# Kernel optimization log

Hardware: AMD Instinct MI355X
Metric: run time of the kernel (lower is better)

Reference implementation:

```python
import jax, jax.numpy as jnp
import numpy as np

B, S, D = 2, 2048, 4096
N_Q_HEADS, N_KV_HEADS, HEAD_DIM = 32, 8, 128
N_REP = N_Q_HEADS // N_KV_HEADS
ROPE_THETA = 10000.0


def setup_inputs() -> dict:
    key = jax.random.key(0)
    ks = jax.random.split(key, 5)
    x = jax.random.normal(ks[0], (B, S, D), dtype=jnp.float32)
    sc = 1.0 / np.sqrt(D)
    wq = jax.random.normal(ks[1], (D, N_Q_HEADS * HEAD_DIM), dtype=jnp.float32) * sc
    wk = jax.random.normal(ks[2], (D, N_KV_HEADS * HEAD_DIM), dtype=jnp.float32) * sc
    wv = jax.random.normal(ks[3], (D, N_KV_HEADS * HEAD_DIM), dtype=jnp.float32) * sc
    cache_k = jnp.zeros((B, S, N_KV_HEADS, HEAD_DIM), dtype=jnp.float32)
    cache_v = jnp.zeros((B, S, N_KV_HEADS, HEAD_DIM), dtype=jnp.float32)
    # rotary frequencies: theta_i = 1/ROPE_THETA^(2i/hd), angle = pos * theta_i
    inv_freq = 1.0 / (ROPE_THETA ** (np.arange(0, HEAD_DIM, 2, dtype=np.float32) / HEAD_DIM))
    angles = np.arange(S, dtype=np.float32)[:, None] * inv_freq[None, :]  # [S, hd/2]
    freqs_cos = jnp.asarray(np.cos(angles), dtype=jnp.float32)
    freqs_sin = jnp.asarray(np.sin(angles), dtype=jnp.float32)
    return {"x": x, "wq": wq, "wk": wk, "wv": wv,
            "cache_k": cache_k, "cache_v": cache_v,
            "freqs_cos": freqs_cos, "freqs_sin": freqs_sin,
            "start_pos": 0}


def _apply_rope(x, cos, sin):
    # x: [B, S, H, hd]; cos/sin: [S, hd/2] -> complex rotation of adjacent pairs
    xr = x[..., 0::2]
    xi = x[..., 1::2]
    c = cos[None, :, None, :]
    s = sin[None, :, None, :]
    out_r = xr * c - xi * s
    out_i = xr * s + xi * c
    return jnp.stack([out_r, out_i], axis=-1).reshape(x.shape)


def reference(x, wq, wk, wv, cache_k, cache_v, freqs_cos, freqs_sin, start_pos):
    batch, seq_len, _ = x.shape
    xq = (x @ wq).reshape(batch, seq_len, N_Q_HEADS, HEAD_DIM)
    xk = (x @ wk).reshape(batch, seq_len, N_KV_HEADS, HEAD_DIM)
    xv = (x @ wv).reshape(batch, seq_len, N_KV_HEADS, HEAD_DIM)
    xq = _apply_rope(xq, freqs_cos, freqs_sin)
    xk = _apply_rope(xk, freqs_cos, freqs_sin)
    # KV-cache append
    cache_k = jax.lax.dynamic_update_slice(cache_k, xk, (0, start_pos, 0, 0))
    cache_v = jax.lax.dynamic_update_slice(cache_v, xv, (0, start_pos, 0, 0))
    keys = cache_k[:, : start_pos + seq_len]    # [B, T, Hkv, hd]
    values = cache_v[:, : start_pos + seq_len]
    # GQA: repeat kv heads to match query heads
    keys = jnp.repeat(keys, N_REP, axis=2)      # [B, T, Hq, hd]
    values = jnp.repeat(values, N_REP, axis=2)
    scale = 1.0 / jnp.sqrt(jnp.asarray(HEAD_DIM, dtype=x.dtype))
    scores = jnp.einsum("bqhd,bkhd->bhqk", xq, keys) * scale
    probs = jax.nn.softmax(scores.astype(jnp.float32), axis=-1).astype(xq.dtype)
    out = jnp.einsum("bhqk,bkhd->bqhd", probs, values)
    return out.reshape(batch, seq_len, N_Q_HEADS * HEAD_DIM)
```

## Files before the change

kernel.cpp:

```cpp
#include <hip/hip_runtime.h>

#define BATCH   2
#define S_LEN   2048
#define D_MODEL 4096
#define HD      128
#define NQH     32
#define NKVH    8

typedef unsigned short ushort_t;
typedef __bf16 bf16x8 __attribute__((ext_vector_type(8)));
typedef float floatx4 __attribute__((ext_vector_type(4)));

#define MFMA16(a, b, c) __builtin_amdgcn_mfma_f32_16x16x32_bf16(a, b, c, 0, 0, 0)

#if __has_builtin(__builtin_amdgcn_exp2f)
#define EXP2(x) __builtin_amdgcn_exp2f(x)
#else
#define EXP2(x) __expf((x) * 0.6931471805599453f)
#endif

__device__ __forceinline__ ushort_t f2b(float f) {
    unsigned int x;
    __builtin_memcpy(&x, &f, 4);
    x += 0x7fff + ((x >> 16) & 1);
    return (ushort_t)(x >> 16);
}

__device__ __forceinline__ void gld16(void* lds, const void* g) {
    __builtin_amdgcn_global_load_lds(
        (const __attribute__((address_space(1))) void*)g,
        (__attribute__((address_space(3))) void*)lds, 16, 0, 0);
}

__global__ __launch_bounds__(256) void conv_x(const float* __restrict__ x,
                                              ushort_t* __restrict__ x0,
                                              ushort_t* __restrict__ x1) {
    const size_t i = ((size_t)blockIdx.x * 256 + threadIdx.x) << 2;
    float4 v = *(const float4*)&x[i];
    ushort4 p;
    p.x = f2b(v.x); p.y = f2b(v.y); p.z = f2b(v.z); p.w = f2b(v.w);
    ushort_t* dst = (i < 8388608) ? x0 : x1;
    *(ushort4*)&dst[i & 8388607] = p;
}

__global__ __launch_bounds__(256) void pack_w(const float* __restrict__ wq,
                                              const float* __restrict__ wk,
                                              const float* __restrict__ wv,
                                              ushort_t* __restrict__ WT) {
    __shared__ ushort_t t[64][65];
    const int k0 = blockIdx.x << 6;
    const int n0 = blockIdx.y << 6;
    const float* src;
    int scol, sN;
    if (n0 < 4096)      { src = wq; scol = n0;        sN = 4096; }
    else if (n0 < 5120) { src = wk; scol = n0 - 4096; sN = 1024; }
    else                { src = wv; scol = n0 - 5120; sN = 1024; }
    const int tid = threadIdx.x;
#pragma unroll
    for (int i = 0; i < 16; i++) {
        int idx = tid + (i << 8);
        int r = idx >> 6, c = idx & 63;
        t[r][c] = f2b(src[(size_t)(k0 + r) * sN + scol + c]);
    }
    __syncthreads();
#pragma unroll
    for (int i = 0; i < 16; i++) {
        int idx = tid + (i << 8);
        int r = idx >> 6, c = idx & 63;
        WT[(size_t)(n0 + r) * D_MODEL + k0 + c] = t[c][r];
    }
}

__global__ __launch_bounds__(256) void gemm_qkv(const ushort_t* __restrict__ x0,
                                                const ushort_t* __restrict__ x1,
                                                const ushort_t* __restrict__ WT,
                                                const float* __restrict__ fc,
                                                const float* __restrict__ fs,
                                                ushort_t* __restrict__ Qr,
                                                ushort_t* __restrict__ Kr,
                                                ushort_t* __restrict__ Vt) {
    __shared__ ushort_t At[128 * 64];
    __shared__ ushort_t Bt[128 * 64];
    const int tid  = threadIdx.x;
    const int wid  = tid >> 6;
    const int lane = tid & 63;
    const int bm = blockIdx.y << 7;
    const int bn = blockIdx.x << 7;
    const int wm = (wid & 1) << 6;
    const int wn = (wid >> 1) << 6;

    floatx4 acc[4][4] = {};

    const ushort_t* Xb = (bm < 2048) ? x0 : x1;
    const int bml = bm & 2047;

    const int g = (lane & 7) ^ (lane >> 3);
    const ushort_t* gA = Xb + (size_t)(bml + (wid << 5) + (lane >> 3)) * D_MODEL + (g << 3);
    const ushort_t* gB = WT + (size_t)(bn  + (wid << 5) + (lane >> 3)) * D_MODEL + (g << 3);
    ushort_t* lA = &At[wid << 11];
    ushort_t* lB = &Bt[wid << 11];
    const int l7 = lane & 7;
    const int cl = lane & 15, rg = lane >> 4;

    for (int k0 = 0; k0 < D_MODEL; k0 += 64) {
        __syncthreads();
#pragma unroll
        for (int i = 0; i < 4; i++) {
            gld16(lA + (i << 9), gA + (size_t)(i << 3) * D_MODEL + k0);
            gld16(lB + (i << 9), gB + (size_t)(i << 3) * D_MODEL + k0);
        }
        __syncthreads();
#pragma unroll
        for (int kk = 0; kk < 2; kk++) {
            const int c = (kk << 2) + rg;
            const int slot = (c ^ l7) << 3;
            bf16x8 af[4], bfr[4];
#pragma unroll
            for (int mm = 0; mm < 4; mm++) {
                af[mm]  = *(const bf16x8*)&At[((wm + (mm << 4) + cl) << 6) + slot];
                bfr[mm] = *(const bf16x8*)&Bt[((wn + (mm << 4) + cl) << 6) + slot];
            }
#pragma unroll
            for (int mm = 0; mm < 4; mm++)
#pragma unroll
                for (int nn = 0; nn < 4; nn++)
                    acc[mm][nn] = MFMA16(af[mm], bfr[nn], acc[mm][nn]);
        }
    }

    const int region = blockIdx.x;
    const int b_idx  = bm >> 11;
    const int s0w    = (bm & 2047) + wm;

    if (region < 40) {
        const float oscale = (region < 32)
            ? (0.08838834764831845f * 1.4426950408889634f) : 1.0f;
        ushort_t* dst;
        if (region < 32) dst = Qr + (size_t)(b_idx * NQH  +  region      ) * S_LEN * HD;
        else             dst = Kr + (size_t)(b_idx * NKVH + (region - 32)) * S_LEN * HD;
#pragma unroll
        for (int nn = 0; nn < 4; nn++) {
            const int dcol = wn + (nn << 4) + cl;
            const int d2   = dcol >> 1;
            const float sgn = (dcol & 1) ? 1.0f : -1.0f;
#pragma unroll
            for (int mm = 0; mm < 4; mm++)
#pragma unroll
                for (int r = 0; r < 4; r++) {
                    float v  = acc[mm][nn][r];
                    float pv = __shfl_xor(v, 1);
                    int srow = s0w + (mm << 4) + (rg << 2) + r;
                    float c  = fc[(srow << 6) + d2];
                    float s  = fs[(srow << 6) + d2];
                    float o  = (v * c + sgn * pv * s) * oscale;
                    dst[(size_t)srow * HD + dcol] = f2b(o);
                }
        }
    } else {
        const int kvh = region - 40;
        ushort_t* dst = Vt + (size_t)(b_idx * NKVH + kvh) * HD * S_LEN;
#pragma unroll
        for (int mm = 0; mm < 4; mm++) {
            const int srow = s0w + (mm << 4) + (rg << 2);
#pragma unroll
            for (int nn = 0; nn < 4; nn++) {
                const int dcol = wn + (nn << 4) + cl;
                ushort4 pk;
                pk.x = f2b(acc[mm][nn][0]);
                pk.y = f2b(acc[mm][nn][1]);
                pk.z = f2b(acc[mm][nn][2]);
                pk.w = f2b(acc[mm][nn][3]);
                *(ushort4*)&dst[(size_t)dcol * S_LEN + srow] = pk;
            }
        }
    }
}

__global__ __launch_bounds__(256, 3) void attn(const ushort_t* __restrict__ Qr,
                                               const ushort_t* __restrict__ Kr,
                                               const ushort_t* __restrict__ Vtg,
                                               float* __restrict__ out) {
    __shared__ ushort_t Ktb[2][32 * 128];
    __shared__ ushort_t Vlb[2][128 * 32];
    __shared__ ushort_t Pt[4 * 32 * 40];

    const int tid  = threadIdx.x;
    const int wid  = tid >> 6;
    const int lane = tid & 63;
    const int h  = blockIdx.y;
    const int b  = blockIdx.z;
    const int kh = h >> 2;
    const int q0 = (blockIdx.x << 7) + (wid << 5);

    const int cl = lane & 15, rg = lane >> 4, l7 = lane & 7;

    const ushort_t* Qbase = Qr + ((size_t)(b * NQH + h) * S_LEN + q0 + cl) * HD;
    bf16x8 qf0[4], qf1[4];
#pragma unroll
    for (int dc = 0; dc < 4; dc++) {
        qf0[dc] = *(const bf16x8*)&Qbase[(dc << 5) + (rg << 3)];
        qf1[dc] = *(const bf16x8*)&Qbase[(size_t)16 * HD + (dc << 5) + (rg << 3)];
    }

    floatx4 o0[8] = {}, o1[8] = {};
    float ls0[4] = {0.f, 0.f, 0.f, 0.f};
    float ls1[4] = {0.f, 0.f, 0.f, 0.f};

    const ushort_t* Kb = Kr  + (size_t)(b * NKVH + kh) * S_LEN * HD;
    const ushort_t* Vb = Vtg + (size_t)(b * NKVH + kh) * HD * S_LEN;
    ushort_t* Pw = &Pt[wid * 32 * 40];

    const int vr  = lane >> 2;
    const int gv2 = (lane & 3) ^ (vr & 3);

    auto stage = [&](int bi, int kt0) {
#pragma unroll
        for (int i = 0; i < 2; i++) {
            int ki = (wid << 1) + i;
            gld16(&Ktb[bi][ki << 9],
                  Kb + (size_t)(kt0 + (ki << 2) + rg) * HD
                     + ((cl ^ (((ki & 1) << 2) + rg)) << 3));
            gld16(&Vlb[bi][ki << 9],
                  Vb + (size_t)((ki << 4) + vr) * S_LEN + kt0 + (gv2 << 3));
        }
    };

    stage(0, 0);

#pragma unroll 1
    for (int t = 0; t < 64; t++) {
        if (t < 63) {
            stage((t + 1) & 1, (t + 1) << 5);
            asm volatile("s_waitcnt vmcnt(4)" ::: "memory");
        } else {
            asm volatile("s_waitcnt vmcnt(0)" ::: "memory");
        }
        __builtin_amdgcn_s_barrier();
        asm volatile("" ::: "memory");

        const ushort_t* Kc = Ktb[t & 1];
        const ushort_t* Vc = Vlb[t & 1];

        __builtin_amdgcn_s_setprio(1);
#pragma unroll
        for (int kt = 0; kt < 2; kt++) {
            floatx4 a0 = {0.f, 0.f, 0.f, 0.f};
            floatx4 a1 = {0.f, 0.f, 0.f, 0.f};
#pragma unroll
            for (int dc = 0; dc < 4; dc++) {
                int c = (dc << 2) + rg;
                bf16x8 kf = *(const bf16x8*)
                    &Kc[(((kt << 4) + cl) << 7) + ((c ^ l7) << 3)];
                a0 = MFMA16(qf0[dc], kf, a0);
                a1 = MFMA16(qf1[dc], kf, a1);
            }
#pragma unroll
            for (int r = 0; r < 4; r++) {
                float p0 = EXP2(a0[r]);
                float p1 = EXP2(a1[r]);
                ls0[r] += p0;
                ls1[r] += p1;
                Pw[(((rg << 2) + r)     ) * 40 + (kt << 4) + cl] = f2b(p0);
                Pw[(((rg << 2) + r) + 16) * 40 + (kt << 4) + cl] = f2b(p1);
            }
        }

        {
            bf16x8 pf0 = *(const bf16x8*)&Pw[ cl       * 40 + (rg << 3)];
            bf16x8 pf1 = *(const bf16x8*)&Pw[(cl + 16) * 40 + (rg << 3)];
#pragma unroll
            for (int dt = 0; dt < 8; dt++) {
                int d = (dt << 4) + cl;
                bf16x8 vf = *(const bf16x8*)
                    &Vc[(d << 5) + ((rg ^ (cl & 3)) << 3)];
                o0[dt] = MFMA16(pf0, vf, o0[dt]);
                o1[dt] = MFMA16(pf1, vf, o1[dt]);
            }
        }
        __builtin_amdgcn_s_setprio(0);

        asm volatile("" ::: "memory");
        __builtin_amdgcn_s_barrier();
    }

#pragma unroll
    for (int r = 0; r < 4; r++) {
        float v0 = ls0[r];
        v0 += __shfl_xor(v0, 1);
        v0 += __shfl_xor(v0, 2);
        v0 += __shfl_xor(v0, 4);
        v0 += __shfl_xor(v0, 8);
        ls0[r] = 1.0f / v0;
        float v1 = ls1[r];
        v1 += __shfl_xor(v1, 1);
        v1 += __shfl_xor(v1, 2);
        v1 += __shfl_xor(v1, 4);
        v1 += __shfl_xor(v1, 8);
        ls1[r] = 1.0f / v1;
    }

    float* ob = out + (size_t)(b * S_LEN + q0) * (NQH * HD) + h * HD;
#pragma unroll
    for (int dt = 0; dt < 8; dt++)
#pragma unroll
        for (int r = 0; r < 4; r++) {
            ob[(size_t)((rg << 2) + r) * (NQH * HD) + (dt << 4) + cl] =
                o0[dt][r] * ls0[r];
            ob[(size_t)((rg << 2) + r + 16) * (NQH * HD) + (dt << 4) + cl] =
                o1[dt][r] * ls1[r];
        }
}

extern "C" void kernel_launch(void* const* d_in, const int* in_sizes, int n_in,
                              void* d_out, int out_size, void* d_ws, size_t ws_size,
                              hipStream_t stream) {
    const float* x  = (const float*)d_in[0];
    const float* wq = (const float*)d_in[1];
    const float* wk = (const float*)d_in[2];
    const float* wv = (const float*)d_in[3];
    ushort_t* x0 = (ushort_t*)d_in[4];
    ushort_t* x1 = (ushort_t*)d_in[5];
    const float* fc = (const float*)d_in[6];
    const float* fs = (const float*)d_in[7];
    float* out = (float*)d_out;

    ushort_t* WTx = (ushort_t*)d_in[0];

    char* ws = (char*)d_ws;
    ushort_t* Qr = (ushort_t*)(ws);
    ushort_t* Kr = (ushort_t*)(ws + 33554432);
    ushort_t* Vt = (ushort_t*)(ws + 41943040);

    conv_x  <<<16384,           256, 0, stream>>>(x, x0, x1);
    pack_w  <<<dim3(64, 96),    256, 0, stream>>>(wq, wk, wv, WTx);
    gemm_qkv<<<dim3(48, 32),    256, 0, stream>>>(x0, x1, WTx, fc, fs, Qr, Kr, Vt);
    attn    <<<dim3(16, 32, 2), 256, 0, stream>>>(Qr, Kr, Vt, out);
    (void)in_sizes; (void)n_in; (void)out_size; (void)ws_size;
}
```

Measured before the change: 614.8 us.

## Rewrite QKV GEMM as 256x256 tiles with double-buffered LDS pipeline

The QKV projection GEMM moves from 128x128 tiles with 256 threads to 256x256 tiles with 512 threads (8 waves, each computing 128x64). The LDS buffers are now double-buffered so the next K-slice's global-to-LDS loads are issued in stages while the current slice is being multiplied. Raw barriers, vmcnt waits and s_setprio calls schedule this overlap. The aim is to raise arithmetic intensity and hide memory latency. In exchange it uses 128KB of LDS and many more accumulator registers, and launches only 384 blocks, which reduces occupancy and the number of waves in flight.

```diff
diff --git a/kernel.cpp b/kernel.cpp
--- a/kernel.cpp
+++ b/kernel.cpp
@@ -71,85 +71,168 @@
     }
 }
 
-__global__ __launch_bounds__(256) void gemm_qkv(const ushort_t* __restrict__ x0,
-                                                const ushort_t* __restrict__ x1,
-                                                const ushort_t* __restrict__ WT,
-                                                const float* __restrict__ fc,
-                                                const float* __restrict__ fs,
-                                                ushort_t* __restrict__ Qr,
-                                                ushort_t* __restrict__ Kr,
-                                                ushort_t* __restrict__ Vt) {
-    __shared__ ushort_t At[128 * 64];
-    __shared__ ushort_t Bt[128 * 64];
+__global__ __launch_bounds__(512, 2) void gemm_qkv(const ushort_t* __restrict__ x0,
+                                                   const ushort_t* __restrict__ x1,
+                                                   const ushort_t* __restrict__ WT,
+                                                   const float* __restrict__ fc,
+                                                   const float* __restrict__ fs,
+                                                   ushort_t* __restrict__ Qr,
+                                                   ushort_t* __restrict__ Kr,
+                                                   ushort_t* __restrict__ Vt) {
+    __shared__ ushort_t At[2][256 * 64];
+    __shared__ ushort_t Bt[2][256 * 64];
+
     const int tid  = threadIdx.x;
     const int wid  = tid >> 6;
     const int lane = tid & 63;
-    const int bm = blockIdx.y << 7;
-    const int bn = blockIdx.x << 7;
-    const int wm = (wid & 1) << 6;
-    const int wn = (wid >> 1) << 6;
-
-    floatx4 acc[4][4] = {};
+    const int wm = (wid >> 2) << 7;
+    const int wn = (wid & 3) << 6;
+    const int bm = blockIdx.y << 8;
+    const int bn = blockIdx.x << 8;
+    const int cl = lane & 15, rg = lane >> 4, l7 = lane & 7;
 
     const ushort_t* Xb = (bm < 2048) ? x0 : x1;
     const int bml = bm & 2047;
 
-    const int g = (lane & 7) ^ (lane >> 3);
-    const ushort_t* gA = Xb + (size_t)(bml + (wid << 5) + (lane >> 3)) * D_MODEL + (g << 3);
-    const ushort_t* gB = WT + (size_t)(bn  + (wid << 5) + (lane >> 3)) * D_MODEL + (g << 3);
-    ushort_t* lA = &At[wid << 11];
-    ushort_t* lB = &Bt[wid << 11];
-    const int l7 = lane & 7;
-    const int cl = lane & 15, rg = lane >> 4;
-
-    for (int k0 = 0; k0 < D_MODEL; k0 += 64) {
-        __syncthreads();
+    const int srow8 = tid >> 3;
+    const int gsw   = (tid & 7) ^ (srow8 & 7);
+    const ushort_t* gA = Xb + (size_t)(bml + srow8) * D_MODEL + (gsw << 3);
+    const ushort_t* gB = WT + (size_t)(bn  + srow8) * D_MODEL + (gsw << 3);
+    const int lbase = (wid << 3) << 6;
+
+    floatx4 acc[8][4] = {};
+    bf16x8 af[4][2], bfr[4][2];
+
+    auto stA = [&](int buf, int t, int half) {
+#pragma unroll
+        for (int j = 0; j < 2; j++) {
+            const int row0 = (half << 7) + (j << 6);
+            gld16(&At[buf][(row0 << 6) + lbase],
+                  gA + (size_t)row0 * D_MODEL + ((size_t)t << 6));
+        }
+    };
+    auto stB = [&](int buf, int t, int half) {
+#pragma unroll
+        for (int j = 0; j < 2; j++) {
+            const int row0 = (half << 7) + (j << 6);
+            gld16(&Bt[buf][(row0 << 6) + lbase],
+                  gB + (size_t)row0 * D_MODEL + ((size_t)t << 6));
+        }
+    };
+    auto loadA = [&](const ushort_t* buf, int mh) {
 #pragma unroll
         for (int i = 0; i < 4; i++) {
-            gld16(lA + (i << 9), gA + (size_t)(i << 3) * D_MODEL + k0);
-            gld16(lB + (i << 9), gB + (size_t)(i << 3) * D_MODEL + k0);
-        }
-        __syncthreads();
-#pragma unroll
-        for (int kk = 0; kk < 2; kk++) {
-            const int c = (kk << 2) + rg;
-            const int slot = (c ^ l7) << 3;
-            bf16x8 af[4], bfr[4];
-#pragma unroll
-            for (int mm = 0; mm < 4; mm++) {
-                af[mm]  = *(const bf16x8*)&At[((wm + (mm << 4) + cl) << 6) + slot];
-                bfr[mm] = *(const bf16x8*)&Bt[((wn + (mm << 4) + cl) << 6) + slot];
-            }
-#pragma unroll
-            for (int mm = 0; mm < 4; mm++)
-#pragma unroll
-                for (int nn = 0; nn < 4; nn++)
-                    acc[mm][nn] = MFMA16(af[mm], bfr[nn], acc[mm][nn]);
-        }
-    }
-
-    const int region = blockIdx.x;
+            const int row = wm + (mh << 6) + (i << 4) + cl;
+#pragma unroll
+            for (int kk = 0; kk < 2; kk++)
+                af[i][kk] = *(const bf16x8*)
+                    &buf[(row << 6) + ((((kk << 2) + rg) ^ l7) << 3)];
+        }
+    };
+    auto loadB = [&](const ushort_t* buf) {
+#pragma unroll
+        for (int i = 0; i < 4; i++) {
+            const int row = wn + (i << 4) + cl;
+#pragma unroll
+            for (int kk = 0; kk < 2; kk++)
+                bfr[i][kk] = *(const bf16x8*)
+                    &buf[(row << 6) + ((((kk << 2) + rg) ^ l7) << 3)];
+        }
+    };
+
+    stA(0, 0, 0); stA(0, 0, 1); stB(0, 0, 0); stB(0, 0, 1);
+
+#pragma unroll 1
+    for (int t = 0; t < 64; t++) {
+        const int d = t & 1, e = d ^ 1;
+        const ushort_t* Ad = At[d];
+        const ushort_t* Bd = Bt[d];
+
+        if (t < 63) {
+            stA(e, t + 1, 0); stA(e, t + 1, 1);
+            asm volatile("s_waitcnt vmcnt(4)" ::: "memory");
+        } else {
+            asm volatile("s_waitcnt vmcnt(0)" ::: "memory");
+        }
+        __builtin_amdgcn_s_barrier();
+        asm volatile("" ::: "memory");
+        loadA(Ad, 0);
+        loadB(Bd);
+        __builtin_amdgcn_s_setprio(1);
+#pragma unroll
+        for (int i = 0; i < 4; i++)
+#pragma unroll
+            for (int j = 0; j < 2; j++)
+#pragma unroll
+                for (int kk = 0; kk < 2; kk++)
+                    acc[i][j] = MFMA16(af[i][kk], bfr[j][kk], acc[i][j]);
+        __builtin_amdgcn_s_setprio(0);
+        asm volatile("" ::: "memory");
+        __builtin_amdgcn_s_barrier();
+
+        if (t < 63) stB(e, t + 1, 0);
+        __builtin_amdgcn_s_setprio(1);
+#pragma unroll
+        for (int i = 0; i < 4; i++)
+#pragma unroll
+            for (int j = 0; j < 2; j++)
+#pragma unroll
+                for (int kk = 0; kk < 2; kk++)
+                    acc[i][2 + j] = MFMA16(af[i][kk], bfr[2 + j][kk], acc[i][2 + j]);
+        __builtin_amdgcn_s_setprio(0);
+        asm volatile("" ::: "memory");
+        __builtin_amdgcn_s_barrier();
+
+        if (t < 63) stB(e, t + 1, 1);
+        loadA(Ad, 1);
+        __builtin_amdgcn_s_setprio(1);
+#pragma unroll
+        for (int i = 0; i < 4; i++)
+#pragma unroll
+            for (int j = 0; j < 2; j++)
+#pragma unroll
+                for (int kk = 0; kk < 2; kk++)
+                    acc[4 + i][j] = MFMA16(af[i][kk], bfr[j][kk], acc[4 + i][j]);
+        __builtin_amdgcn_s_setprio(0);
+        asm volatile("" ::: "memory");
+        __builtin_amdgcn_s_barrier();
+
+        __builtin_amdgcn_s_setprio(1);
+#pragma unroll
+        for (int i = 0; i < 4; i++)
+#pragma unroll
+            for (int j = 0; j < 2; j++)
+#pragma unroll
+                for (int kk = 0; kk < 2; kk++)
+                    acc[4 + i][2 + j] = MFMA16(af[i][kk], bfr[2 + j][kk], acc[4 + i][2 + j]);
+        __builtin_amdgcn_s_setprio(0);
+        asm volatile("" ::: "memory");
+        __builtin_amdgcn_s_barrier();
+    }
+
     const int b_idx  = bm >> 11;
-    const int s0w    = (bm & 2047) + wm;
-
-    if (region < 40) {
-        const float oscale = (region < 32)
+    const int s_base = (bm & 2047) + wm;
+    const int col0   = bn + wn;
+    const int dbase  = col0 & 127;
+
+    if (col0 < 5120) {
+        const float oscale = (col0 < 4096)
             ? (0.08838834764831845f * 1.4426950408889634f) : 1.0f;
-        ushort_t* dst;
-        if (region < 32) dst = Qr + (size_t)(b_idx * NQH  +  region      ) * S_LEN * HD;
-        else             dst = Kr + (size_t)(b_idx * NKVH + (region - 32)) * S_LEN * HD;
-#pragma unroll
-        for (int nn = 0; nn < 4; nn++) {
-            const int dcol = wn + (nn << 4) + cl;
+        ushort_t* dst = (col0 < 4096)
+            ? Qr + (size_t)(b_idx * NQH  + (col0 >> 7)) * S_LEN * HD
+            : Kr + (size_t)(b_idx * NKVH + ((col0 - 4096) >> 7)) * S_LEN * HD;
+#pragma unroll
+        for (int fn = 0; fn < 4; fn++) {
+            const int dcol = dbase + (fn << 4) + cl;
             const int d2   = dcol >> 1;
             const float sgn = (dcol & 1) ? 1.0f : -1.0f;
 #pragma unroll
-            for (int mm = 0; mm < 4; mm++)
+            for (int fm = 0; fm < 8; fm++)
 #pragma unroll
                 for (int r = 0; r < 4; r++) {
-                    float v  = acc[mm][nn][r];
+                    float v  = acc[fm][fn][r];
                     float pv = __shfl_xor(v, 1);
-                    int srow = s0w + (mm << 4) + (rg << 2) + r;
+                    int srow = s_base + (fm << 4) + (rg << 2) + r;
                     float c  = fc[(srow << 6) + d2];
                     float s  = fs[(srow << 6) + d2];
                     float o  = (v * c + sgn * pv * s) * oscale;
@@ -157,19 +240,19 @@
                 }
         }
     } else {
-        const int kvh = region - 40;
+        const int kvh = (col0 - 5120) >> 7;
         ushort_t* dst = Vt + (size_t)(b_idx * NKVH + kvh) * HD * S_LEN;
 #pragma unroll
-        for (int mm = 0; mm < 4; mm++) {
-            const int srow = s0w + (mm << 4) + (rg << 2);
-#pragma unroll
-            for (int nn = 0; nn < 4; nn++) {
-                const int dcol = wn + (nn << 4) + cl;
+        for (int fm = 0; fm < 8; fm++) {
+            const int srow = s_base + (fm << 4) + (rg << 2);
+#pragma unroll
+            for (int fn = 0; fn < 4; fn++) {
+                const int dcol = dbase + (fn << 4) + cl;
                 ushort4 pk;
-                pk.x = f2b(acc[mm][nn][0]);
-                pk.y = f2b(acc[mm][nn][1]);
-                pk.z = f2b(acc[mm][nn][2]);
-                pk.w = f2b(acc[mm][nn][3]);
+                pk.x = f2b(acc[fm][fn][0]);
+                pk.y = f2b(acc[fm][fn][1]);
+                pk.z = f2b(acc[fm][fn][2]);
+                pk.w = f2b(acc[fm][fn][3]);
                 *(ushort4*)&dst[(size_t)dcol * S_LEN + srow] = pk;
             }
         }
@@ -333,7 +416,7 @@
 
     conv_x  <<<16384,           256, 0, stream>>>(x, x0, x1);
     pack_w  <<<dim3(64, 96),    256, 0, stream>>>(wq, wk, wv, WTx);
-    gemm_qkv<<<dim3(48, 32),    256, 0, stream>>>(x0, x1, WTx, fc, fs, Qr, Kr, Vt);
+    gemm_qkv<<<dim3(24, 16),    512, 0, stream>>>(x0, x1, WTx, fc, fs, Qr, Kr, Vt);
     attn    <<<dim3(16, 32, 2), 256, 0, stream>>>(Qr, Kr, Vt, out);
     (void)in_sizes; (void)n_in; (void)out_size; (void)ws_size;
 }
```

Result: slower. 650.0 us (+5.7%).
